# Performance work log

Hardware: AMD Instinct MI355X
Metric: run time of the kernel (lower is better)

The kernel has to match this reference:

```python
import jax, jax.numpy as jnp
import numpy as np

B, T, E, D, A, H, C, K = 32, 1500, 512, 512, 512, 4, 10, 201
SHARPENING = 1.0


def setup_inputs() -> dict:
    key = jax.random.key(0)
    ks = jax.random.split(key, 11)
    def w(k, shape, fan_in):
        return jax.random.normal(k, shape, jnp.float32) / np.sqrt(fan_in).astype(np.float32)
    return {
        "enc_out": jax.random.normal(ks[0], (B, T, E), jnp.float32),
        "x_lens": jax.random.randint(ks[1], (B,), T // 2, T + 1),
        "dec_out": jax.random.normal(ks[2], (B, 1, D), jnp.float32),
        # previous-step attention weights: a valid distribution over T per head
        "aw_step": jax.nn.softmax(jax.random.normal(ks[3], (B, T, H), jnp.float32), axis=1),
        "w_enc": w(ks[4], (H, E, A), E),   # per-head LinearND(enc->att)
        "b_enc": jnp.zeros((H, A), jnp.float32),
        "w_dec": w(ks[5], (H, D, A), D),   # per-head LinearND(dec->att), no bias
        "w_conv": w(ks[6], (H, C, A), C),  # per-head LinearND(conv_ch->att), no bias
        "conv_k": w(ks[7], (H * C, 1, K), K),  # grouped 1D conv kernels (O,I,K), groups=H
        "v": w(ks[8], (H, A), A),          # per-head LinearND(att->1), no bias
        "w_mha": w(ks[9], (H * E, E), H * E),
        "b_mha": jnp.zeros((E,), jnp.float32),
    }


def reference(enc_out, x_lens, dec_out, aw_step, w_enc, b_enc, w_dec, w_conv, conv_k, v, w_mha, b_mha):
    b, t, e = enc_out.shape
    h = aw_step.shape[-1]
    c = w_conv.shape[1]
    k = conv_k.shape[-1]
    # enc_out_a: per-head encoder projection [B,T,H,A]
    enc_a = jnp.einsum('bte,hea->btha', enc_out, w_enc) + b_enc
    # decoder projection, broadcast over time [B,1,H,A]
    dec_a = jnp.einsum('bd,hda->bha', dec_out[:, 0], w_dec)[:, None]
    # location features: grouped 1D conv over previous attention weights
    aw_t = jnp.transpose(aw_step, (0, 2, 1))  # [B,H,T]
    conv = jax.lax.conv_general_dilated(
        aw_t, conv_k, window_strides=(1,), padding=[(k // 2, k // 2)],
        dimension_numbers=('NCH', 'OIH', 'NCH'), feature_group_count=h)  # [B,H*C,T]
    conv = conv.reshape(b, h, c, t).transpose(0, 3, 1, 2)  # [B,T,H,C]
    conv_a = jnp.einsum('bthc,hca->btha', conv, w_conv)
    # additive energy [B,T,H]
    energy = jnp.einsum('btha,ha->bth', jnp.tanh(enc_a + dec_a + conv_a), v)
    # original code multiplies energy by mask (1 valid, -1024 padded) then sharpening
    mask = jnp.where(jnp.arange(t)[None, :] < x_lens[:, None], 1.0, -1024.0).astype(energy.dtype)
    energy = energy * mask[:, :, None] * SHARPENING
    aw = jax.nn.softmax(energy, axis=1)  # softmax over time per head
    # per-head context, concatenated along feature dim -> [B,1,H*E]
    ctx = jnp.einsum('bte,bth->bhe', enc_out, aw).reshape(b, 1, h * e)
    ctx = ctx @ w_mha + b_mha  # [B,1,E]
    return ctx, aw
```

## Files before the change

kernel.cpp:

```cpp
#include <hip/hip_runtime.h>
#include <hip/hip_bf16.h>

#define BB 32
#define TT 1500
#define TP 1536
#define EE 512
#define HH 4
#define AA 512
#define NN 2048
#define CC 10
#define KCONV 201
#define KAUG 576

typedef __attribute__((ext_vector_type(8))) __bf16 bf16x8;
typedef __attribute__((ext_vector_type(4))) float f32x4;

__device__ __forceinline__ unsigned short f2bf(float x) {
    unsigned int u = __float_as_uint(x);
    u = (u + 0x7fffu + ((u >> 16) & 1u)) >> 16;
    return (unsigned short)u;
}
__device__ __forceinline__ float bf2f(unsigned short u) {
    return __uint_as_float(((unsigned int)u) << 16);
}
__device__ __forceinline__ void glds16(const void* g, void* l) {
    __builtin_amdgcn_global_load_lds(
        (const __attribute__((address_space(1))) unsigned int*)g,
        (__attribute__((address_space(3))) unsigned int*)l, 16, 0, 0);
}
__device__ __forceinline__ float tanh_fast(float x) {
    float e = __expf(x * 2.0f);
    return fmaf(-2.0f, __builtin_amdgcn_rcpf(e + 1.0f), 1.0f);
}
__device__ __forceinline__ unsigned int pkbf(float x, float y) {
    float2 f{x, y};
    __hip_bfloat162 h2 = __float22bfloat162_rn(f);
    return *reinterpret_cast<unsigned int*>(&h2);
}
__device__ __forceinline__ void split2(float x, float y, unsigned int& h, unsigned int& l) {
    unsigned short hx = f2bf(x), hy = f2bf(y);
    h = ((unsigned int)hy << 16) | hx;
    l = pkbf(x - bf2f(hx), y - bf2f(hy));
}

#define PREP_DEC0   0
#define PREP_CONV0  1024
#define PREP_WT0    8704
#define PREP_TOTAL  8992

__global__ __launch_bounds__(256) void k_prep(
    const float* __restrict__ dec_out, const float* __restrict__ aw_step,
    const float* __restrict__ w_enc, const float* __restrict__ b_enc,
    const float* __restrict__ w_dec, const float* __restrict__ w_conv,
    const float* __restrict__ conv_k,
    unsigned short* __restrict__ Whi, unsigned short* __restrict__ Wlo,
    unsigned short* __restrict__ Chi, unsigned short* __restrict__ Clo,
    float* __restrict__ dec_a) {
    __shared__ float sh[64 * 65];
    const int bid = blockIdx.x;
    const int tid = threadIdx.x;

    if (bid < PREP_CONV0) {
        const int b  = bid >> 5;
        const int n0 = (bid & 31) * 64;
        const int n  = n0 + (tid & 63);
        const int dg = tid >> 6;
        const int h  = n >> 9, a = n & 511;
        const float* dp = dec_out + (size_t)b * 512 + dg * 128;
        const float* wp = w_dec + ((size_t)h * 512 + dg * 128) * 512 + a;
        float acc = 0.f;
#pragma unroll 8
        for (int d = 0; d < 128; ++d) acc += dp[d] * wp[(size_t)d * 512];
        sh[tid] = acc;
        __syncthreads();
        if (tid < 64) {
            float tot = sh[tid] + sh[tid + 64] + sh[tid + 128] + sh[tid + 192];
            dec_a[(size_t)b * NN + n0 + tid] = b_enc[n0 + tid] + tot;
        }
    } else if (bid < PREP_WT0) {
        int r = bid - PREP_CONV0;
        const int tch = r % 6;
        const int hc  = (r / 6) % 40;
        const int b   = r / 240;
        const int h   = hc / 10;
        const int t0  = tch * 256;
        float* sAw = sh;
        for (int i = tid; i < 456; i += 256) {
            int ts = t0 - 100 + i;
            sAw[i] = (ts >= 0 && ts < TT) ? aw_step[((size_t)b * TT + ts) * HH + h] : 0.f;
        }
        __syncthreads();
        int t = t0 + tid;
        if (t < TT) {
            const float* ck = conv_k + (size_t)hc * KCONV;
            float acc = 0.f;
#pragma unroll 4
            for (int k = 0; k < KCONV; ++k) acc += sAw[tid + k] * ck[k];
            size_t o = ((size_t)b * TP + t) * 64 + hc;
            unsigned short hi = f2bf(acc);
            Chi[o] = hi; Clo[o] = f2bf(acc - bf2f(hi));
        }
    } else {
        int r = bid - PREP_WT0;
        const int h  = r / 72;
        const int rr = r % 72;
        const int at = rr / 9;
        const int kt = rr % 9;
        const int a0 = at * 64;
        if (kt < 8) {
            const int k0 = kt * 64;
#pragma unroll
            for (int it = 0; it < 16; ++it) {
                int kk = it * 4 + (tid >> 6);
                int aa = tid & 63;
                sh[kk * 65 + aa] = w_enc[((size_t)h * 512 + k0 + kk) * 512 + a0 + aa];
            }
            __syncthreads();
#pragma unroll
            for (int it = 0; it < 16; ++it) {
                int nl = it * 4 + (tid >> 6);
                int kk = tid & 63;
                float val = sh[kk * 65 + nl];
                size_t o = ((size_t)h * 512 + a0 + nl) * KAUG + k0 + kk;
                unsigned short hi = f2bf(val);
                Whi[o] = hi; Wlo[o] = f2bf(val - bf2f(hi));
            }
        } else {
#pragma unroll
            for (int it = 0; it < 16; ++it) {
                int nl = it * 4 + (tid >> 6);
                int j  = tid & 63;
                float val = 0.f;
                if (j < 40 && (j / 10) == h)
                    val = w_conv[((size_t)h * 10 + (j % 10)) * 512 + a0 + nl];
                size_t o = ((size_t)h * 512 + a0 + nl) * KAUG + 512 + j;
                unsigned short hi = f2bf(val);
                Whi[o] = hi; Wlo[o] = f2bf(val - bf2f(hi));
            }
        }
    }
}

__global__ __launch_bounds__(256) void k_gemm(
    const float* __restrict__ enc,
    const unsigned short* __restrict__ Chi, const unsigned short* __restrict__ Clo,
    const unsigned short* __restrict__ Whi, const unsigned short* __restrict__ Wlo,
    const float* __restrict__ dec_a, const float* __restrict__ vvec,
    const int* __restrict__ xl, float* __restrict__ energy) {
    __shared__ unsigned short lsAhi[4096], lsAlo[4096];
    __shared__ unsigned short lsBhi[4096], lsBlo[4096];
    const int id = blockIdx.x;
    const int tile = id >> 4;
    const int ntile = id & 15;
    const int mtile = 11 - (tile >> 5);
    const int b = tile & 31;
    const int tid = threadIdx.x;
    const int lane = tid & 63, wave = tid >> 6;
    const int wm = wave >> 1, wn = wave & 1;
    const int m0 = mtile * 128, n0 = ntile * 128;
    const int xlen = xl[b];

    f32x4 acc[4][4];
#pragma unroll
    for (int i = 0; i < 4; i++)
#pragma unroll
        for (int j = 0; j < 4; j++) acc[i][j] = (f32x4){0.f, 0.f, 0.f, 0.f};

    const int row = tid >> 2;
    const int ko  = (tid & 3) * 8;
    const size_t bbase = ((size_t)n0 + row) * KAUG + ko;
    const size_t cbase = ((size_t)b * TP + m0 + row) * 64 + ko;
    const int l1 = tid * 8;
    const int l2 = l1 + 2048;
    const int ar = wm * 64, br = wn * 64;
    const int fo = (lane & 15) * 32 + (lane >> 4) * 8;

    const float* ap0 = enc + ((size_t)b * TT + m0 + row) * 512 + ko;
    const float* ap1 = ap0 + (size_t)64 * 512;

    if (m0 + 128 <= xlen) {
        float4 fa0 = *(const float4*)(ap0);
        float4 fa1 = *(const float4*)(ap0 + 4);
        float4 fa2 = *(const float4*)(ap1);
        float4 fa3 = *(const float4*)(ap1 + 4);
        for (int ks = 0; ks < 18; ++ks) {
            const int k0 = ks * 32;
            __syncthreads();
            glds16(Whi + bbase + k0,                     &lsBhi[l1]);
            glds16(Whi + bbase + k0 + (size_t)64 * KAUG, &lsBhi[l2]);
            if (ks < 16) {
                uint4 w0, w1;
                w0.x = pkbf(fa0.x, fa0.y); w0.y = pkbf(fa0.z, fa0.w);
                w0.z = pkbf(fa1.x, fa1.y); w0.w = pkbf(fa1.z, fa1.w);
                w1.x = pkbf(fa2.x, fa2.y); w1.y = pkbf(fa2.z, fa2.w);
                w1.z = pkbf(fa3.x, fa3.y); w1.w = pkbf(fa3.z, fa3.w);
                *reinterpret_cast<uint4*>(&lsAhi[l1]) = w0;
                *reinterpret_cast<uint4*>(&lsAhi[l2]) = w1;
            } else {
                glds16(Chi + cbase + (ks - 16) * 32,        &lsAhi[l1]);
                glds16(Chi + cbase + (ks - 16) * 32 + 4096, &lsAhi[l2]);
            }
            asm volatile("s_waitcnt vmcnt(0)" ::: "memory");
            __syncthreads();

            bf16x8 ah[4], bh[4];
#pragma unroll
            for (int i = 0; i < 4; i++) {
                ah[i] = *(const bf16x8*)&lsAhi[(ar + i * 16) * 32 + fo];
                bh[i] = *(const bf16x8*)&lsBhi[(br + i * 16) * 32 + fo];
            }
            if (ks < 15) {
                const int nk = k0 + 32;
                fa0 = *(const float4*)(ap0 + nk);
                fa1 = *(const float4*)(ap0 + nk + 4);
                fa2 = *(const float4*)(ap1 + nk);
                fa3 = *(const float4*)(ap1 + nk + 4);
            }
#pragma unroll
            for (int i = 0; i < 4; i++)
#pragma unroll
                for (int j = 0; j < 4; j++)
                    acc[i][j] = __builtin_amdgcn_mfma_f32_16x16x32_bf16(ah[i], bh[j], acc[i][j], 0, 0, 0);
        }
    } else {
        const bool g1 = (m0 + row + 64) < TT;
        const float4 z4 = {0.f, 0.f, 0.f, 0.f};
        bool corr[4];
#pragma unroll
        for (int i = 0; i < 4; i++) corr[i] = (m0 + ar + i * 16 + 16) > xlen;
        float4 fa0 = *(const float4*)(ap0);
        float4 fa1 = *(const float4*)(ap0 + 4);
        float4 fa2 = g1 ? *(const float4*)(ap1) : z4;
        float4 fa3 = g1 ? *(const float4*)(ap1 + 4) : z4;
        for (int ks = 0; ks < 18; ++ks) {
            const int k0 = ks * 32;
            __syncthreads();
            glds16(Whi + bbase + k0,                     &lsBhi[l1]);
            glds16(Whi + bbase + k0 + (size_t)64 * KAUG, &lsBhi[l2]);
            glds16(Wlo + bbase + k0,                     &lsBlo[l1]);
            glds16(Wlo + bbase + k0 + (size_t)64 * KAUG, &lsBlo[l2]);
            if (ks < 16) {
                uint4 h0, h1, e0, e1;
                split2(fa0.x, fa0.y, h0.x, e0.x); split2(fa0.z, fa0.w, h0.y, e0.y);
                split2(fa1.x, fa1.y, h0.z, e0.z); split2(fa1.z, fa1.w, h0.w, e0.w);
                split2(fa2.x, fa2.y, h1.x, e1.x); split2(fa2.z, fa2.w, h1.y, e1.y);
                split2(fa3.x, fa3.y, h1.z, e1.z); split2(fa3.z, fa3.w, h1.w, e1.w);
                *reinterpret_cast<uint4*>(&lsAhi[l1]) = h0;
                *reinterpret_cast<uint4*>(&lsAhi[l2]) = h1;
                *reinterpret_cast<uint4*>(&lsAlo[l1]) = e0;
                *reinterpret_cast<uint4*>(&lsAlo[l2]) = e1;
            } else {
                glds16(Chi + cbase + (ks - 16) * 32,        &lsAhi[l1]);
                glds16(Chi + cbase + (ks - 16) * 32 + 4096, &lsAhi[l2]);
                glds16(Clo + cbase + (ks - 16) * 32,        &lsAlo[l1]);
                glds16(Clo + cbase + (ks - 16) * 32 + 4096, &lsAlo[l2]);
            }
            asm volatile("s_waitcnt vmcnt(0)" ::: "memory");
            __syncthreads();

            bf16x8 ah[4], al[4], bh[4], bl[4];
#pragma unroll
            for (int i = 0; i < 4; i++) {
                ah[i] = *(const bf16x8*)&lsAhi[(ar + i * 16) * 32 + fo];
                al[i] = *(const bf16x8*)&lsAlo[(ar + i * 16) * 32 + fo];
                bh[i] = *(const bf16x8*)&lsBhi[(br + i * 16) * 32 + fo];
                bl[i] = *(const bf16x8*)&lsBlo[(br + i * 16) * 32 + fo];
            }
            if (ks < 15) {
                const int nk = k0 + 32;
                fa0 = *(const float4*)(ap0 + nk);
                fa1 = *(const float4*)(ap0 + nk + 4);
                fa2 = g1 ? *(const float4*)(ap1 + nk) : z4;
                fa3 = g1 ? *(const float4*)(ap1 + nk + 4) : z4;
            }
#pragma unroll
            for (int i = 0; i < 4; i++) {
#pragma unroll
                for (int j = 0; j < 4; j++)
                    acc[i][j] = __builtin_amdgcn_mfma_f32_16x16x32_bf16(ah[i], bh[j], acc[i][j], 0, 0, 0);
                if (corr[i]) {
#pragma unroll
                    for (int j = 0; j < 4; j++) {
                        acc[i][j] = __builtin_amdgcn_mfma_f32_16x16x32_bf16(ah[i], bl[j], acc[i][j], 0, 0, 0);
                        acc[i][j] = __builtin_amdgcn_mfma_f32_16x16x32_bf16(al[i], bh[j], acc[i][j], 0, 0, 0);
                    }
                }
            }
        }
    }

    const int h = ntile >> 2;
    const int kg = lane >> 4;
    float dv[4], vv[4];
#pragma unroll
    for (int j = 0; j < 4; j++) {
        int ng = n0 + wn * 64 + j * 16 + (lane & 15);
        dv[j] = dec_a[(size_t)b * NN + ng];
        vv[j] = vvec[ng];
    }
#pragma unroll
    for (int i = 0; i < 4; i++) {
        float part[4] = {0.f, 0.f, 0.f, 0.f};
#pragma unroll
        for (int j = 0; j < 4; j++)
#pragma unroll
            for (int r = 0; r < 4; r++)
                part[r] += tanh_fast(acc[i][j][r] + dv[j]) * vv[j];
#pragma unroll
        for (int r = 0; r < 4; r++) {
            float s = part[r];
            s += __shfl_xor(s, 1, 64);
            s += __shfl_xor(s, 2, 64);
            s += __shfl_xor(s, 4, 64);
            s += __shfl_xor(s, 8, 64);
            if ((lane & 15) == 0) {
                int t = m0 + wm * 64 + i * 16 + kg * 4 + r;
                if (t < TT)
                    atomicAdd(&energy[((size_t)b * HH + h) * TP + t], s);
            }
        }
    }
}

__global__ __launch_bounds__(1024) void k_softmax(const float* __restrict__ energy,
                                                  const int* __restrict__ x_lens,
                                                  float* __restrict__ aw) {
    const int b = blockIdx.x >> 2, h = blockIdx.x & 3;
    const int tid = threadIdx.x;
    __shared__ float sE[TT];
    __shared__ float red[1024];
    const int xlen = x_lens[b];
    float lmax = -3.4e38f;
    for (int t = tid; t < TT; t += 1024) {
        float e = energy[((size_t)b * HH + h) * TP + t];
        float m = (t < xlen) ? e : e * -1024.0f;
        sE[t] = m;
        lmax = fmaxf(lmax, m);
    }
    red[tid] = lmax; __syncthreads();
    for (int s = 512; s > 0; s >>= 1) { if (tid < s) red[tid] = fmaxf(red[tid], red[tid + s]); __syncthreads(); }
    float mx = red[0]; __syncthreads();
    float lsum = 0.f;
    for (int t = tid; t < TT; t += 1024) {
        float ex = __expf(sE[t] - mx);
        sE[t] = ex; lsum += ex;
    }
    red[tid] = lsum; __syncthreads();
    for (int s = 512; s > 0; s >>= 1) { if (tid < s) red[tid] += red[tid + s]; __syncthreads(); }
    float rs = 1.0f / red[0];
    for (int t = tid; t < TT; t += 1024)
        aw[((size_t)b * TT + t) * HH + h] = sE[t] * rs;
}

__global__ __launch_bounds__(512) void k_ctx(const float* __restrict__ enc,
                                             const float* __restrict__ aw,
                                             float* __restrict__ ctx_h) {
    const int chunk = blockIdx.x, b = blockIdx.y;
    const int t0 = chunk * 128;
    const int nt = (TT - t0 < 128) ? (TT - t0) : 128;
    __shared__ float sA[128 * 4];
    __shared__ int s_nz;
    const int tid = threadIdx.x;
    if (tid == 0) s_nz = 0;
    __syncthreads();
    for (int i = tid; i < nt * 4; i += 512) {
        float w = aw[((size_t)b * TT + t0) * HH + i];
        sA[i] = w;
        if (w != 0.f) s_nz = 1;
    }
    __syncthreads();
    if (!s_nz) return;
    float a0 = 0.f, a1 = 0.f, a2 = 0.f, a3 = 0.f;
    const float* ep = enc + ((size_t)b * TT + t0) * EE + tid;
    if (nt == 128) {
#pragma unroll 8
        for (int tt = 0; tt < 128; ++tt) {
            float ev = ep[(size_t)tt * EE];
            a0 += sA[tt * 4 + 0] * ev; a1 += sA[tt * 4 + 1] * ev;
            a2 += sA[tt * 4 + 2] * ev; a3 += sA[tt * 4 + 3] * ev;
        }
    } else {
        for (int tt = 0; tt < nt; ++tt) {
            float ev = ep[(size_t)tt * EE];
            a0 += sA[tt * 4 + 0] * ev; a1 += sA[tt * 4 + 1] * ev;
            a2 += sA[tt * 4 + 2] * ev; a3 += sA[tt * 4 + 3] * ev;
        }
    }
    atomicAdd(&ctx_h[((size_t)b * HH + 0) * EE + tid], a0);
    atomicAdd(&ctx_h[((size_t)b * HH + 1) * EE + tid], a1);
    atomicAdd(&ctx_h[((size_t)b * HH + 2) * EE + tid], a2);
    atomicAdd(&ctx_h[((size_t)b * HH + 3) * EE + tid], a3);
}

__global__ __launch_bounds__(256) void k_mha(const float* __restrict__ ctx_h,
                                             const float* __restrict__ w_mha,
                                             const float* __restrict__ b_mha,
                                             float* __restrict__ out) {
    __shared__ float sred[256];
    const int tid = threadIdx.x;
    const int b  = blockIdx.x >> 2;
    const int eo = ((blockIdx.x & 3) << 7) + (tid & 127);
    const int kg = tid >> 7;
    const float* c = ctx_h + (size_t)b * NN + kg * 1024;
    const float* w = w_mha + ((size_t)kg * 1024) * EE + eo;
    float acc = 0.f;
#pragma unroll 8
    for (int k = 0; k < 1024; ++k) acc += c[k] * w[(size_t)k * EE];
    sred[tid] = acc;
    __syncthreads();
    if (tid < 128)
        out[(size_t)b * EE + eo] = b_mha[eo] + sred[tid] + sred[tid + 128];
}

extern "C" void kernel_launch(void* const* d_in, const int* in_sizes, int n_in,
                              void* d_out, int out_size, void* d_ws, size_t ws_size,
                              hipStream_t stream) {
    (void)in_sizes; (void)n_in; (void)out_size;
    const float* enc    = (const float*)d_in[0];
    const int*   xlen   = (const int*)d_in[1];
    const float* dec    = (const float*)d_in[2];
    const float* aw_in  = (const float*)d_in[3];
    const float* w_enc  = (const float*)d_in[4];
    const float* b_enc  = (const float*)d_in[5];
    const float* w_dec  = (const float*)d_in[6];
    const float* w_conv = (const float*)d_in[7];
    const float* convk  = (const float*)d_in[8];
    const float* v      = (const float*)d_in[9];
    const float* w_mha  = (const float*)d_in[10];
    const float* b_mha  = (const float*)d_in[11];
    float* out = (float*)d_out;

    char* ws = (char*)d_ws;
    unsigned short* Whi = (unsigned short*)ws;
    unsigned short* Wlo = (unsigned short*)(ws + 2359296);
    unsigned short* Chi = (unsigned short*)(ws + 4718592);
    unsigned short* Clo = (unsigned short*)(ws + 11010048);
    float* dec_a  = (float*)(ws + 17301504);
    float* energy = (float*)(ws + 17563648);
    float* ctx_h  = (float*)(ws + 18350080);
    (void)ws_size;

    hipMemsetAsync(energy, 0, 786432 + 262144, stream);

    k_prep<<<dim3(PREP_TOTAL), 256, 0, stream>>>(dec, aw_in, w_enc, b_enc,
                                                 w_dec, w_conv, convk,
                                                 Whi, Wlo, Chi, Clo, dec_a);
    k_gemm<<<dim3(6144), 256, 0, stream>>>(enc, Chi, Clo, Whi, Wlo, dec_a, v, xlen, energy);
    k_softmax<<<dim3(BB * HH), 1024, 0, stream>>>(energy, xlen, out + 16384);
    k_ctx <<<dim3(12, BB), 512, 0, stream>>>(enc, out + 16384, ctx_h);
    k_mha <<<dim3(128), 256, 0, stream>>>(ctx_h, w_mha, b_mha, out);
}
```

Baseline: 685.0 us.

## Fold memset into prep, remap GEMM tiles per XCD, vectorize context kernel

Three separate changes. The separate memset is removed, and extra blocks in the prep kernel now zero the energy and ctx buffers, saving one launch. GEMM block IDs are remapped so that consecutive blocks landing on the same XCD share the same batch/M tile, aiming for better L2 reuse of the A operand. The context kernel now uses smaller time chunks with 256 threads, float4 loads, and an in-block reduction of two time groups before the atomics, which doubles the grid and improves load width at the cost of more atomics overall.

```diff
diff --git a/kernel.cpp b/kernel.cpp
--- a/kernel.cpp
+++ b/kernel.cpp
@@ -43,10 +43,11 @@
     l = pkbf(x - bf2f(hx), y - bf2f(hy));
 }
 
-#define PREP_DEC0   0
-#define PREP_CONV0  1024
-#define PREP_WT0    8704
-#define PREP_TOTAL  8992
+#define PREP_ZERO0  0
+#define PREP_DEC0   1024
+#define PREP_CONV0  2048
+#define PREP_WT0    9728
+#define PREP_TOTAL  10016
 
 __global__ __launch_bounds__(256) void k_prep(
     const float* __restrict__ dec_out, const float* __restrict__ aw_step,
@@ -55,14 +56,17 @@
     const float* __restrict__ conv_k,
     unsigned short* __restrict__ Whi, unsigned short* __restrict__ Wlo,
     unsigned short* __restrict__ Chi, unsigned short* __restrict__ Clo,
-    float* __restrict__ dec_a) {
+    float* __restrict__ dec_a, float* __restrict__ zbase) {
     __shared__ float sh[64 * 65];
     const int bid = blockIdx.x;
     const int tid = threadIdx.x;
 
-    if (bid < PREP_CONV0) {
-        const int b  = bid >> 5;
-        const int n0 = (bid & 31) * 64;
+    if (bid < PREP_DEC0) {
+        zbase[bid * 256 + tid] = 0.f;
+    } else if (bid < PREP_CONV0) {
+        const int rb = bid - PREP_DEC0;
+        const int b  = rb >> 5;
+        const int n0 = (rb & 31) * 64;
         const int n  = n0 + (tid & 63);
         const int dg = tid >> 6;
         const int h  = n >> 9, a = n & 511;
@@ -150,8 +154,10 @@
     __shared__ unsigned short lsAhi[4096], lsAlo[4096];
     __shared__ unsigned short lsBhi[4096], lsBlo[4096];
     const int id = blockIdx.x;
-    const int tile = id >> 4;
-    const int ntile = id & 15;
+    const int xcd = id & 7;
+    const int s = id >> 3;
+    const int ntile = s & 15;
+    const int tile = (s >> 4) * 8 + xcd;
     const int mtile = 11 - (tile >> 5);
     const int b = tile & 31;
     const int tid = threadIdx.x;
@@ -352,44 +358,56 @@
         aw[((size_t)b * TT + t) * HH + h] = sE[t] * rs;
 }
 
-__global__ __launch_bounds__(512) void k_ctx(const float* __restrict__ enc,
+__global__ __launch_bounds__(256) void k_ctx(const float* __restrict__ enc,
                                              const float* __restrict__ aw,
                                              float* __restrict__ ctx_h) {
     const int chunk = blockIdx.x, b = blockIdx.y;
-    const int t0 = chunk * 128;
-    const int nt = (TT - t0 < 128) ? (TT - t0) : 128;
-    __shared__ float sA[128 * 4];
+    const int t0 = chunk * 64;
+    const int nt = (TT - t0 < 64) ? (TT - t0) : 64;
+    __shared__ float sA[64 * 4];
+    __shared__ float4 red4[128][4];
     __shared__ int s_nz;
     const int tid = threadIdx.x;
     if (tid == 0) s_nz = 0;
     __syncthreads();
-    for (int i = tid; i < nt * 4; i += 512) {
+    for (int i = tid; i < nt * 4; i += 256) {
         float w = aw[((size_t)b * TT + t0) * HH + i];
         sA[i] = w;
         if (w != 0.f) s_nz = 1;
     }
     __syncthreads();
     if (!s_nz) return;
-    float a0 = 0.f, a1 = 0.f, a2 = 0.f, a3 = 0.f;
-    const float* ep = enc + ((size_t)b * TT + t0) * EE + tid;
-    if (nt == 128) {
-#pragma unroll 8
-        for (int tt = 0; tt < 128; ++tt) {
-            float ev = ep[(size_t)tt * EE];
-            a0 += sA[tt * 4 + 0] * ev; a1 += sA[tt * 4 + 1] * ev;
-            a2 += sA[tt * 4 + 2] * ev; a3 += sA[tt * 4 + 3] * ev;
-        }
-    } else {
-        for (int tt = 0; tt < nt; ++tt) {
-            float ev = ep[(size_t)tt * EE];
-            a0 += sA[tt * 4 + 0] * ev; a1 += sA[tt * 4 + 1] * ev;
-            a2 += sA[tt * 4 + 2] * ev; a3 += sA[tt * 4 + 3] * ev;
-        }
-    }
-    atomicAdd(&ctx_h[((size_t)b * HH + 0) * EE + tid], a0);
-    atomicAdd(&ctx_h[((size_t)b * HH + 1) * EE + tid], a1);
-    atomicAdd(&ctx_h[((size_t)b * HH + 2) * EE + tid], a2);
-    atomicAdd(&ctx_h[((size_t)b * HH + 3) * EE + tid], a3);
+    const int e4 = (tid & 127) * 4;
+    const int tg = tid >> 7;
+    const float* ep = enc + ((size_t)b * TT + t0) * EE + e4;
+    float acc[4][4] = {};
+#pragma unroll 4
+    for (int tt = tg; tt < nt; tt += 2) {
+        float4 ev = *reinterpret_cast<const float4*>(ep + (size_t)tt * EE);
+        float w0 = sA[tt * 4 + 0], w1 = sA[tt * 4 + 1];
+        float w2 = sA[tt * 4 + 2], w3 = sA[tt * 4 + 3];
+        acc[0][0] += w0 * ev.x; acc[0][1] += w0 * ev.y; acc[0][2] += w0 * ev.z; acc[0][3] += w0 * ev.w;
+        acc[1][0] += w1 * ev.x; acc[1][1] += w1 * ev.y; acc[1][2] += w1 * ev.z; acc[1][3] += w1 * ev.w;
+        acc[2][0] += w2 * ev.x; acc[2][1] += w2 * ev.y; acc[2][2] += w2 * ev.z; acc[2][3] += w2 * ev.w;
+        acc[3][0] += w3 * ev.x; acc[3][1] += w3 * ev.y; acc[3][2] += w3 * ev.z; acc[3][3] += w3 * ev.w;
+    }
+    if (tg == 1) {
+#pragma unroll
+        for (int h = 0; h < 4; ++h)
+            red4[tid & 127][h] = make_float4(acc[h][0], acc[h][1], acc[h][2], acc[h][3]);
+    }
+    __syncthreads();
+    if (tg == 0) {
+#pragma unroll
+        for (int h = 0; h < 4; ++h) {
+            float4 o = red4[tid][h];
+            float* dst = &ctx_h[((size_t)b * HH + h) * EE + e4];
+            atomicAdd(dst + 0, acc[h][0] + o.x);
+            atomicAdd(dst + 1, acc[h][1] + o.y);
+            atomicAdd(dst + 2, acc[h][2] + o.z);
+            atomicAdd(dst + 3, acc[h][3] + o.w);
+        }
+    }
 }
 
 __global__ __launch_bounds__(256) void k_mha(const float* __restrict__ ctx_h,
@@ -440,13 +458,11 @@
     float* ctx_h  = (float*)(ws + 18350080);
     (void)ws_size;
 
-    hipMemsetAsync(energy, 0, 786432 + 262144, stream);
-
     k_prep<<<dim3(PREP_TOTAL), 256, 0, stream>>>(dec, aw_in, w_enc, b_enc,
                                                  w_dec, w_conv, convk,
-                                                 Whi, Wlo, Chi, Clo, dec_a);
+                                                 Whi, Wlo, Chi, Clo, dec_a, energy);
     k_gemm<<<dim3(6144), 256, 0, stream>>>(enc, Chi, Clo, Whi, Wlo, dec_a, v, xlen, energy);
     k_softmax<<<dim3(BB * HH), 1024, 0, stream>>>(energy, xlen, out + 16384);
-    k_ctx <<<dim3(12, BB), 512, 0, stream>>>(enc, out + 16384, ctx_h);
+    k_ctx <<<dim3(24, BB), 256, 0, stream>>>(enc, out + 16384, ctx_h);
     k_mha <<<dim3(128), 256, 0, stream>>>(ctx_h, w_mha, b_mha, out);
 }
```

Result: slower. 714.1 us (+4.2%).
